# Kernel optimization log

Measured on AMD Instinct MI355X. Metric: run time of the kernel, lower is better.

The kernel has to match this reference:

```python
import jax, jax.numpy as jnp
import numpy as np

N, E, D = 50000, 800000, 256   # nodes, edges, hidden_dim
H, B, A = 8, 4, 3              # num_heads, num_bases, num_aggregators (symnorm,sum,max)
F = D // H                      # per-head width = bases feature width
G = 64                          # number of graphs in the batch
EPS = 1e-5                      # GraphNorm eps


def setup_inputs() -> dict:
    key = jax.random.key(0)
    ks = jax.random.split(key, 8)
    glorot = lambda k, shape: jax.random.normal(k, shape, jnp.float32) * np.sqrt(2.0 / (shape[0] + shape[1])).astype(np.float32)
    return {
        "node": jax.random.normal(ks[0], (N, D), jnp.float32),
        "edge_attr": jax.random.normal(ks[1], (E, 1), jnp.float32),  # unused by layer, kept for signature fidelity
        "W_bases": glorot(ks[2], (D, B * F)),                 # EGConv bases linear (no bias)
        "W_comb": glorot(ks[3], (D, H * B * A)),              # EGConv combination-weight linear
        "b_comb": jnp.zeros((H * B * A,), jnp.float32),
        "conv_bias": jnp.zeros((D,), jnp.float32),
        "gn_weight": jnp.ones((D,), jnp.float32),             # GraphNorm gamma
        "gn_bias": jnp.zeros((D,), jnp.float32),              # GraphNorm beta
        "gn_mean_scale": jnp.ones((D,), jnp.float32),         # GraphNorm alpha
        "edge_index": jax.random.randint(ks[4], (2, E), 0, N, dtype=jnp.int32),
        "batch": jnp.sort(jax.random.randint(ks[5], (N,), 0, G, dtype=jnp.int32)),
    }


def _forward(node, W_bases, W_comb, b_comb, conv_bias, gn_weight, gn_bias, gn_mean_scale, edge_index, batch):
    n = node.shape[0]
    loops = jnp.arange(n, dtype=edge_index.dtype)
    src = jnp.concatenate([edge_index[0], loops])  # add self-loops (EGConv add_self_loops=True / gcn_norm)
    dst = jnp.concatenate([edge_index[1], loops])

    # gcn_norm symmetric weights deg^-1/2[src] * deg^-1/2[dst]
    deg = jax.ops.segment_sum(jnp.ones_like(src, dtype=node.dtype), dst, num_segments=n)
    dinv = jnp.where(deg > 0, jax.lax.rsqrt(deg), 0.0)
    sym_w = dinv[src] * dinv[dst]

    bases = node @ W_bases            # [N, B*F]
    comb = node @ W_comb + b_comb     # [N, H*B*A]

    msg = bases[src]                  # [E+N, B*F] edge gather (dominant traffic)
    agg_sym = jax.ops.segment_sum(msg * sym_w[:, None], dst, num_segments=n)
    agg_sum = jax.ops.segment_sum(msg, dst, num_segments=n)
    agg_max = jax.ops.segment_max(msg, dst, num_segments=n)  # self-loops guarantee non-empty segments

    aggregated = jnp.stack([agg_sym, agg_sum, agg_max], axis=1)       # [N, A, B*F]
    aggregated = aggregated.reshape(n, A * B, F)                      # (a,b) fused index, as in PyG view
    weightings = comb.reshape(n, H, B * A)
    h = jnp.einsum('nhk,nkf->nhf', weightings, aggregated).reshape(n, D) + conv_bias

    # GraphNorm: per-graph mean/var with learnable mean scale alpha
    counts = jnp.maximum(jax.ops.segment_sum(jnp.ones((n,), node.dtype), batch, num_segments=G), 1.0)
    mean = jax.ops.segment_sum(h, batch, num_segments=G) / counts[:, None]
    hc = h - gn_mean_scale * mean[batch]
    var = jax.ops.segment_sum(hc * hc, batch, num_segments=G) / counts[:, None]
    out = gn_weight * hc * jax.lax.rsqrt(var[batch] + EPS) + gn_bias
    return jax.nn.relu(out)


def reference(node, edge_attr, W_bases, W_comb, b_comb, conv_bias, gn_weight, gn_bias, gn_mean_scale, edge_index, batch):
    del edge_attr  # unused by EGConv_layer, present in the torch forward signature
    return _forward(node, W_bases, W_comb, b_comb, conv_bias, gn_weight, gn_bias, gn_mean_scale, edge_index, batch)
```

## Files before the change

### kernel.cpp

```cpp
#include <hip/hip_runtime.h>
#include <hip/hip_bf16.h>

#define NN 50000
#define EE 800000
#define DD 256
#define BF 128
#define HC 96
#define GG 64
#define NT 14
#define KCN 8
#define RC 98
#define RSH 9
#define RSZ 512
#define CC 256
#define CS 3125
#define CAP 10240
#define SL 8
#define STG 10752

typedef short s16x8 __attribute__((ext_vector_type(8)));
typedef float f32x4 __attribute__((ext_vector_type(4)));

static __device__ __forceinline__ float b2f(unsigned u) {
    unsigned x = u << 16;
    float f;
    __builtin_memcpy(&f, &x, 4);
    return f;
}
static __device__ __forceinline__ unsigned short f2b(float f) {
    unsigned x;
    __builtin_memcpy(&x, &f, 4);
    unsigned lsb = (x >> 16) & 1u;
    x += 0x7fffu + lsb;
    return (unsigned short)(x >> 16);
}
static __device__ __forceinline__ unsigned pack_trunc(float lo, float hi) {
    unsigned ulo, uhi;
    __builtin_memcpy(&ulo, &lo, 4);
    __builtin_memcpy(&uhi, &hi, 4);
    return (ulo >> 16) | (uhi & 0xffff0000u);
}

__global__ void k_setup(const unsigned short* node_u16, int* flag,
                        const void* bcomb, const void* cbias, const void* gw,
                        const void* gb, const void* gms,
                        float* bcombF, float* cbiasF, float* gwF, float* gbF, float* gmsF,
                        const int* batch, int* goff) {
    if (blockIdx.x == 0) {
        __shared__ int cnt;
        if (threadIdx.x == 0) cnt = 0;
        __syncthreads();
        int local = 0;
        #pragma unroll
        for (int j = 0; j < 4; j++) {
            int idx = 2 * (threadIdx.x * 4 + j);
            unsigned short u = node_u16[idx];
            int e = (u >> 7) & 0xFF;
            if (e < 100 || e > 140) local++;
        }
        atomicAdd(&cnt, local);
        __syncthreads();
        int isf = (cnt > 256) ? 1 : 0;
        if (threadIdx.x == 0) flag[0] = isf;
        int d = threadIdx.x;
        auto rd = [&](const void* p, int i) -> float {
            return isf ? ((const float*)p)[i] : b2f(((const unsigned short*)p)[i]);
        };
        if (d < HC) bcombF[d] = rd(bcomb, d);
        cbiasF[d] = rd(cbias, d);
        gwF[d] = rd(gw, d);
        gbF[d] = rd(gb, d);
        gmsF[d] = rd(gms, d);
    } else {
        int g = threadIdx.x;
        if (g > GG) return;
        int lo = 0, hi = NN;
        while (lo < hi) { int mid = (lo + hi) >> 1; if (batch[mid] < g) lo = mid + 1; else hi = mid; }
        goff[g] = lo;
    }
}

__global__ __launch_bounds__(256) void k_cnt(const int* ei, int* cntg) {
    __shared__ int cnt[RC];
    int c = blockIdx.x, t = threadIdx.x;
    if (t < RC) cnt[t] = 0;
    __syncthreads();
    const int* dstp = ei + EE + (size_t)c * CS;
    for (int i = t; i < CS; i += 256) atomicAdd(&cnt[dstp[i] >> RSH], 1);
    __syncthreads();
    if (t < RC) cntg[c * RC + t] = cnt[t];
}

__global__ __launch_bounds__(256) void k_cscan(const int* cntg, int* baseg, int* cntr) {
    __shared__ int lds[256];
    int r = blockIdx.x, t = threadIdx.x;
    int v = cntg[t * RC + r];
    lds[t] = v;
    __syncthreads();
    for (int ofs = 1; ofs < 256; ofs <<= 1) {
        int add = (t >= ofs) ? lds[t - ofs] : 0;
        __syncthreads();
        lds[t] += add;
        __syncthreads();
    }
    baseg[t * RC + r] = r * CAP + lds[t] - v;
    if (t == 255) cntr[r] = lds[255];
}

__global__ void k_rscan(const int* cntr, int* rbase, int* row_off) {
    __shared__ int lds[128];
    int t = threadIdx.x;
    int nr = (t < RC) ? ((t == RC - 1) ? (NN - (RC - 1) * RSZ) : RSZ) : 0;
    int v = (t < RC) ? cntr[t] + nr : 0;
    lds[t] = v;
    __syncthreads();
    for (int ofs = 1; ofs < 128; ofs <<= 1) {
        int add = (t >= ofs) ? lds[t - ofs] : 0;
        __syncthreads();
        lds[t] += add;
        __syncthreads();
    }
    if (t < RC) rbase[t] = lds[t] - v;
    if (t == RC - 1) row_off[NN] = lds[t];
}

__global__ __launch_bounds__(256) void k_bucket(const int* ei, const int* baseg, unsigned* bucket) {
    __shared__ int cur[RC];
    int c = blockIdx.x, t = threadIdx.x;
    if (t < RC) cur[t] = baseg[c * RC + t];
    __syncthreads();
    const int* srcp = ei + (size_t)c * CS;
    const int* dstp = ei + EE + (size_t)c * CS;
    for (int i = t; i < CS; i += 256) {
        int d = dstp[i], s = srcp[i];
        int r = d >> RSH;
        int pos = atomicAdd(&cur[r], 1);
        bucket[pos] = ((unsigned)s << RSH) | (unsigned)(d & (RSZ - 1));
    }
}

__global__ __launch_bounds__(256) void k_build(const unsigned* bucket, const int* cntr,
                                               const int* rbase, int* row_off, float* dinv,
                                               int* csr) {
    __shared__ int hist[RSZ];
    __shared__ int stage[STG];
    __shared__ int scanbuf[256];
    int r = blockIdx.x, t = threadIdx.x;
    int n0 = r * RSZ;
    int nr = NN - n0; if (nr > RSZ) nr = RSZ;
    int cr = cntr[r];
    int rb = rbase[r];
    const unsigned* bk = bucket + (size_t)r * CAP;
    #pragma unroll
    for (int j = 0; j < 2; j++) hist[t + j * 256] = 0;
    __syncthreads();
    for (int i = t; i < cr; i += 256) atomicAdd(&hist[bk[i] & (RSZ - 1)], 1);
    __syncthreads();
    int a0 = (2 * t     < nr) ? hist[2 * t] + 1     : 0;
    int a1 = (2 * t + 1 < nr) ? hist[2 * t + 1] + 1 : 0;
    int s = a0 + a1;
    scanbuf[t] = s;
    __syncthreads();
    for (int ofs = 1; ofs < 256; ofs <<= 1) {
        int add = (t >= ofs) ? scanbuf[t - ofs] : 0;
        __syncthreads();
        scanbuf[t] += add;
        __syncthreads();
    }
    int excl = scanbuf[t] - s;
    int total = scanbuf[255];
    __syncthreads();
    if (2 * t < nr) {
        int n = 2 * t;
        row_off[n0 + n] = rb + excl;
        dinv[n0 + n] = rsqrtf((float)a0);
        stage[excl] = n0 + n;
        hist[n] = excl + 1;
    }
    if (2 * t + 1 < nr) {
        int n = 2 * t + 1;
        int e1 = excl + a0;
        row_off[n0 + n] = rb + e1;
        dinv[n0 + n] = rsqrtf((float)a1);
        stage[e1] = n0 + n;
        hist[n] = e1 + 1;
    }
    __syncthreads();
    for (int i = t; i < cr; i += 256) {
        unsigned p = bk[i];
        int slot = atomicAdd(&hist[p & (RSZ - 1)], 1);
        stage[slot] = (int)(p >> RSH);
    }
    __syncthreads();
    for (int i = t; i < total; i += 256) csr[rb + i] = stage[i];
}

__global__ void k_pack(const int* flag, const void* Wb, const void* Wc, unsigned short* wpack) {
    int t = blockIdx.x, kc = blockIdx.y, lane = threadIdx.x;
    int isf = flag[0];
    int n = t * 16 + (lane & 15);
    int kb = kc * 32 + (lane >> 4) * 8;
    unsigned short* o = wpack + (size_t)(((t * KCN) + kc) * 64 + lane) * 8;
    #pragma unroll
    for (int j = 0; j < 8; j++) {
        int k = kb + j;
        int src = (n < BF) ? (k * BF + n) : (k * HC + (n - BF));
        const void* W = (n < BF) ? Wb : Wc;
        o[j] = isf ? f2b(((const float*)W)[src]) : ((const unsigned short*)W)[src];
    }
}

__global__ __launch_bounds__(256) void k_gemm(const int* flag, const void* node,
                                              const unsigned short* wpack, const float* bcombF,
                                              unsigned short* bases, float* comb) {
    int wv = threadIdx.x >> 6, lane = threadIdx.x & 63;
    int row0 = blockIdx.x * 64 + wv * 16;
    int m = row0 + (lane & 15);
    int mc = m < NN ? m : NN - 1;
    int kg = lane >> 4;
    int isf = flag[0];
    const s16x8* bp = reinterpret_cast<const s16x8*>(wpack);
    f32x4 acc[NT];
    #pragma unroll
    for (int t = 0; t < NT; t++) acc[t] = (f32x4){0.f, 0.f, 0.f, 0.f};
    if (isf) {
        const float* nf = (const float*)node + (size_t)mc * DD;
        for (int kc = 0; kc < KCN; kc++) {
            const f32x4* src = reinterpret_cast<const f32x4*>(nf + kc * 32 + kg * 8);
            f32x4 x0 = src[0], x1 = src[1];
            union { s16x8 v; unsigned u[4]; } a;
            a.u[0] = pack_trunc(x0[0], x0[1]);
            a.u[1] = pack_trunc(x0[2], x0[3]);
            a.u[2] = pack_trunc(x1[0], x1[1]);
            a.u[3] = pack_trunc(x1[2], x1[3]);
            #pragma unroll
            for (int t = 0; t < NT; t++) {
                s16x8 b = bp[(size_t)(t * KCN + kc) * 64 + lane];
                acc[t] = __builtin_amdgcn_mfma_f32_16x16x32_bf16(a.v, b, acc[t], 0, 0, 0);
            }
        }
    } else {
        const s16x8* ap = reinterpret_cast<const s16x8*>(node);
        for (int kc = 0; kc < KCN; kc++) {
            s16x8 a = ap[(size_t)mc * 32 + kc * 4 + kg];
            #pragma unroll
            for (int t = 0; t < NT; t++) {
                s16x8 b = bp[(size_t)(t * KCN + kc) * 64 + lane];
                acc[t] = __builtin_amdgcn_mfma_f32_16x16x32_bf16(a, b, acc[t], 0, 0, 0);
            }
        }
    }
    int colb = lane & 15;
    #pragma unroll
    for (int t = 0; t < NT; t++) {
        int nc = t * 16 + colb;
        #pragma unroll
        for (int i = 0; i < 4; i++) {
            int r = row0 + kg * 4 + i;
            if (r < NN) {
                float v = acc[t][i];
                if (nc < BF) bases[(size_t)r * BF + nc] = f2b(v);
                else comb[(size_t)r * HC + (nc - BF)] = v + bcombF[nc - BF];
            }
        }
    }
}

__global__ __launch_bounds__(256) void k_agg(const unsigned short* bases,
                                             const float* comb, const float* dinv,
                                             const int* row_off, const int* csr,
                                             const float* cbiasF, unsigned short* h) {
    __shared__ float2 lds[4][3][64];
    int wv = threadIdx.x >> 6, lane = threadIdx.x & 63;
    int v = blockIdx.x * 4 + wv;
    int r0 = row_off[v], r1 = row_off[v + 1];
    float dv = dinv[v];
    const unsigned* bp = reinterpret_cast<const unsigned*>(bases);
    float sy0 = 0.f, sy1 = 0.f, su0 = 0.f, su1 = 0.f;
    float mx0 = -3.4e38f, mx1 = -3.4e38f;
    for (int base = r0; base < r1; base += 64) {
        int nload = r1 - base; if (nload > 64) nload = 64;
        int sidx = 0; float wgt = 0.f;
        if (lane < nload) { sidx = csr[base + lane]; wgt = dinv[sidx] * dv; }
        int j = 0;
        for (; j + 4 <= nload; j += 4) {
            int s0 = __shfl(sidx, j),     s1 = __shfl(sidx, j + 1);
            int s2 = __shfl(sidx, j + 2), s3 = __shfl(sidx, j + 3);
            float w0 = __shfl(wgt, j),     w1 = __shfl(wgt, j + 1);
            float w2 = __shfl(wgt, j + 2), w3 = __shfl(wgt, j + 3);
            unsigned g0 = bp[(size_t)s0 * 64 + lane];
            unsigned g1 = bp[(size_t)s1 * 64 + lane];
            unsigned g2 = bp[(size_t)s2 * 64 + lane];
            unsigned g3 = bp[(size_t)s3 * 64 + lane];
            float a, b;
            a = b2f(g0 & 0xffffu); b = b2f(g0 >> 16);
            sy0 += w0 * a; sy1 += w0 * b; su0 += a; su1 += b; mx0 = fmaxf(mx0, a); mx1 = fmaxf(mx1, b);
            a = b2f(g1 & 0xffffu); b = b2f(g1 >> 16);
            sy0 += w1 * a; sy1 += w1 * b; su0 += a; su1 += b; mx0 = fmaxf(mx0, a); mx1 = fmaxf(mx1, b);
            a = b2f(g2 & 0xffffu); b = b2f(g2 >> 16);
            sy0 += w2 * a; sy1 += w2 * b; su0 += a; su1 += b; mx0 = fmaxf(mx0, a); mx1 = fmaxf(mx1, b);
            a = b2f(g3 & 0xffffu); b = b2f(g3 >> 16);
            sy0 += w3 * a; sy1 += w3 * b; su0 += a; su1 += b; mx0 = fmaxf(mx0, a); mx1 = fmaxf(mx1, b);
        }
        for (; j < nload; j++) {
            int s0 = __shfl(sidx, j); float w0 = __shfl(wgt, j);
            unsigned g0 = bp[(size_t)s0 * 64 + lane];
            float a = b2f(g0 & 0xffffu), b = b2f(g0 >> 16);
            sy0 += w0 * a; sy1 += w0 * b; su0 += a; su1 += b; mx0 = fmaxf(mx0, a); mx1 = fmaxf(mx1, b);
        }
    }
    lds[wv][0][lane] = (float2){sy0, sy1};
    lds[wv][1][lane] = (float2){su0, su1};
    lds[wv][2][lane] = (float2){mx0, mx1};
    __syncthreads();
    const float* P0 = (const float*)&lds[wv][0][0];
    const float* P1 = (const float*)&lds[wv][1][0];
    const float* P2 = (const float*)&lds[wv][2][0];
    int d0 = lane * 4;
    int hh = d0 >> 5;
    float cb[12];
    #pragma unroll
    for (int k = 0; k < 12; k++) cb[k] = comb[(size_t)v * HC + hh * 12 + k];
    union { unsigned short e[4]; uint2 u; } o;
    #pragma unroll
    for (int i = 0; i < 4; i++) {
        int d = d0 + i, f = d & 31;
        float acc = cbiasF[d];
        #pragma unroll
        for (int k = 0; k < 12; k++) {
            int a = k >> 2, b = k & 3;
            const float* P = (a == 0) ? P0 : ((a == 1) ? P1 : P2);
            acc += cb[k] * P[b * 32 + f];
        }
        o.e[i] = f2b(acc);
    }
    reinterpret_cast<uint2*>(h)[(size_t)v * 64 + lane] = o.u;
}

__global__ void k_stats1(const unsigned short* h, const int* goff, float* sstat) {
    int g = blockIdx.x, s = blockIdx.y, t = threadIdx.x;
    int v0 = goff[g], v1 = goff[g + 1];
    float sum = 0.f, sq = 0.f;
    for (int v = v0 + s; v < v1; v += SL) {
        float x = b2f(h[(size_t)v * DD + t]);
        sum += x; sq += x * x;
    }
    size_t o = ((size_t)(g * SL + s)) * (2 * DD);
    sstat[o + t] = sum;
    sstat[o + DD + t] = sq;
}

__global__ void k_stats2(const float* sstat, const int* goff,
                         const float* gwF, const float* gbF, const float* gmsF,
                         float* sA, float* sB) {
    int g = blockIdx.x, d = threadIdx.x;
    float sum = 0.f, sq = 0.f;
    #pragma unroll
    for (int s = 0; s < SL; s++) {
        size_t o = ((size_t)(g * SL + s)) * (2 * DD);
        sum += sstat[o + d];
        sq  += sstat[o + DD + d];
    }
    int c = goff[g + 1] - goff[g];
    float cnt = (float)(c > 1 ? c : 1);
    float mu = sum / cnt;
    float m2 = sq / cnt;
    float al = gmsF[d];
    float var = m2 - mu * mu * (2.f * al - al * al);
    float rstd = rsqrtf(var + 1e-5f);
    float sa = gwF[d] * rstd;
    sA[g * DD + d] = sa;
    sB[g * DD + d] = gbF[d] - sa * al * mu;
}

__global__ void k_out(const int* flag, const unsigned short* h, const int* batch,
                      const float* sA, const float* sB, void* out) {
    int tid = blockIdx.x * 256 + threadIdx.x;
    int v = tid >> 6, q = tid & 63;
    if (v >= NN) return;
    int g = batch[v];
    uint2 xr = reinterpret_cast<const uint2*>(h)[(size_t)v * 64 + q];
    f32x4 a = reinterpret_cast<const f32x4*>(sA)[g * 64 + q];
    f32x4 b = reinterpret_cast<const f32x4*>(sB)[g * 64 + q];
    float x0 = b2f(xr.x & 0xffffu), x1 = b2f(xr.x >> 16);
    float x2 = b2f(xr.y & 0xffffu), x3 = b2f(xr.y >> 16);
    float y0 = fmaxf(x0 * a[0] + b[0], 0.f);
    float y1 = fmaxf(x1 * a[1] + b[1], 0.f);
    float y2 = fmaxf(x2 * a[2] + b[2], 0.f);
    float y3 = fmaxf(x3 * a[3] + b[3], 0.f);
    if (flag[0]) {
        f32x4 y = {y0, y1, y2, y3};
        reinterpret_cast<f32x4*>(out)[(size_t)v * 64 + q] = y;
    } else {
        union { unsigned short e[4]; uint2 u; } o;
        o.e[0] = f2b(y0); o.e[1] = f2b(y1); o.e[2] = f2b(y2); o.e[3] = f2b(y3);
        reinterpret_cast<uint2*>(out)[(size_t)v * 64 + q] = o.u;
    }
}

extern "C" void kernel_launch(void* const* d_in, const int* in_sizes, int n_in,
                              void* d_out, int out_size, void* d_ws, size_t ws_size,
                              hipStream_t stream) {
    const void* node  = d_in[0];
    const void* Wb    = d_in[2];
    const void* Wc    = d_in[3];
    const void* bcomb = d_in[4];
    const void* cbias = d_in[5];
    const void* gw    = d_in[6];
    const void* gb    = d_in[7];
    const void* gms   = d_in[8];
    const int* ei     = (const int*)d_in[9];
    const int* batch  = (const int*)d_in[10];

    char* w = (char*)d_ws;
    size_t off = 0;
    auto alloc = [&](size_t bytes) -> void* {
        off = (off + 255) & ~(size_t)255;
        void* p = w + off;
        off += bytes;
        return p;
    };
    unsigned short* bases = (unsigned short*)alloc((size_t)NN * BF * 2);
    float* comb    = (float*)alloc((size_t)NN * HC * 4);
    unsigned short* h = (unsigned short*)alloc((size_t)NN * DD * 2);
    int*   csr     = (int*)alloc((size_t)(EE + NN) * 4);
    unsigned* bucket = (unsigned*)alloc((size_t)RC * CAP * 4);
    int*   cntg    = (int*)alloc((size_t)CC * RC * 4);
    int*   baseg   = (int*)alloc((size_t)CC * RC * 4);
    int*   cntrr   = (int*)alloc((size_t)RC * 4);
    int*   rbase   = (int*)alloc((size_t)RC * 4);
    float* dinv    = (float*)alloc((size_t)NN * 4);
    int*   row_off = (int*)alloc((size_t)(NN + 1) * 4);
    int*   goff    = (int*)alloc((size_t)(GG + 1) * 4);
    float* sstat   = (float*)alloc((size_t)GG * SL * 2 * DD * 4);
    float* sA      = (float*)alloc((size_t)GG * DD * 4);
    float* sB      = (float*)alloc((size_t)GG * DD * 4);
    unsigned short* wpack = (unsigned short*)alloc((size_t)NT * KCN * 64 * 8 * 2);
    int*   flag    = (int*)alloc(256);
    float* bcombF  = (float*)alloc(HC * 4);
    float* cbiasF  = (float*)alloc(DD * 4);
    float* gwF     = (float*)alloc(DD * 4);
    float* gbF     = (float*)alloc(DD * 4);
    float* gmsF    = (float*)alloc(DD * 4);

    k_setup<<<2, 256, 0, stream>>>((const unsigned short*)node, flag, bcomb, cbias, gw, gb, gms,
                                   bcombF, cbiasF, gwF, gbF, gmsF, batch, goff);
    k_cnt<<<CC, 256, 0, stream>>>(ei, cntg);
    k_cscan<<<RC, 256, 0, stream>>>(cntg, baseg, cntrr);
    k_rscan<<<1, 128, 0, stream>>>(cntrr, rbase, row_off);
    k_bucket<<<CC, 256, 0, stream>>>(ei, baseg, bucket);
    k_build<<<RC, 256, 0, stream>>>(bucket, cntrr, rbase, row_off, dinv, csr);
    k_pack<<<dim3(NT, KCN), 64, 0, stream>>>(flag, Wb, Wc, wpack);
    k_gemm<<<(NN + 63) / 64, 256, 0, stream>>>(flag, node, wpack, bcombF, bases, comb);
    k_agg<<<NN / 4, 256, 0, stream>>>(bases, comb, dinv, row_off, csr, cbiasF, h);
    k_stats1<<<dim3(GG, SL), 256, 0, stream>>>(h, goff, sstat);
    k_stats2<<<GG, 256, 0, stream>>>(sstat, goff, gwF, gbF, gmsF, sA, sB);
    k_out<<<(NN * 64 + 255) / 256, 256, 0, stream>>>(flag, h, batch, sA, sB, d_out);
}
```

Measured before the change: 271.2 us.

## Retile GEMM across waves, widen gather unroll, vectorize GraphNorm stats

The GEMM kernel now gives each block 16 rows, with two waves each computing 7 of the 14 output column tiles. This cuts accumulator registers and raises the block count. The aggregation loop is unrolled to issue 8 independent row gathers before accumulating, which puts more memory loads in flight. The stats pass reads two bf16 values per thread with half as many threads, and the graph split factor is doubled to 16 for more parallelism. The row bounds checks are dropped because N divides evenly by 16. The node A-tile is now loaded twice per block, once per wave.

New measurement: 267.9 us. No clear change (-1.2%).

```diff
diff --git a/kernel.cpp b/kernel.cpp
--- a/kernel.cpp
+++ b/kernel.cpp
@@ -15,7 +15,7 @@
 #define CC 256
 #define CS 3125
 #define CAP 10240
-#define SL 8
+#define SL 16
 #define STG 10752
 
 typedef short s16x8 __attribute__((ext_vector_type(8)));
@@ -210,21 +210,19 @@
     }
 }
 
-__global__ __launch_bounds__(256) void k_gemm(const int* flag, const void* node,
+__global__ __launch_bounds__(128) void k_gemm(const int* flag, const void* node,
                                               const unsigned short* wpack, const float* bcombF,
                                               unsigned short* bases, float* comb) {
     int wv = threadIdx.x >> 6, lane = threadIdx.x & 63;
-    int row0 = blockIdx.x * 64 + wv * 16;
-    int m = row0 + (lane & 15);
-    int mc = m < NN ? m : NN - 1;
+    int m = blockIdx.x * 16 + (lane & 15);
     int kg = lane >> 4;
     int isf = flag[0];
     const s16x8* bp = reinterpret_cast<const s16x8*>(wpack);
-    f32x4 acc[NT];
-    #pragma unroll
-    for (int t = 0; t < NT; t++) acc[t] = (f32x4){0.f, 0.f, 0.f, 0.f};
+    f32x4 acc[7];
+    #pragma unroll
+    for (int t = 0; t < 7; t++) acc[t] = (f32x4){0.f, 0.f, 0.f, 0.f};
     if (isf) {
-        const float* nf = (const float*)node + (size_t)mc * DD;
+        const float* nf = (const float*)node + (size_t)m * DD;
         for (int kc = 0; kc < KCN; kc++) {
             const f32x4* src = reinterpret_cast<const f32x4*>(nf + kc * 32 + kg * 8);
             f32x4 x0 = src[0], x1 = src[1];
@@ -234,34 +232,35 @@
             a.u[2] = pack_trunc(x1[0], x1[1]);
             a.u[3] = pack_trunc(x1[2], x1[3]);
             #pragma unroll
-            for (int t = 0; t < NT; t++) {
+            for (int t2 = 0; t2 < 7; t2++) {
+                int t = wv * 7 + t2;
                 s16x8 b = bp[(size_t)(t * KCN + kc) * 64 + lane];
-                acc[t] = __builtin_amdgcn_mfma_f32_16x16x32_bf16(a.v, b, acc[t], 0, 0, 0);
+                acc[t2] = __builtin_amdgcn_mfma_f32_16x16x32_bf16(a.v, b, acc[t2], 0, 0, 0);
             }
         }
     } else {
         const s16x8* ap = reinterpret_cast<const s16x8*>(node);
         for (int kc = 0; kc < KCN; kc++) {
-            s16x8 a = ap[(size_t)mc * 32 + kc * 4 + kg];
+            s16x8 a = ap[(size_t)m * 32 + kc * 4 + kg];
             #pragma unroll
-            for (int t = 0; t < NT; t++) {
+            for (int t2 = 0; t2 < 7; t2++) {
+                int t = wv * 7 + t2;
                 s16x8 b = bp[(size_t)(t * KCN + kc) * 64 + lane];
-                acc[t] = __builtin_amdgcn_mfma_f32_16x16x32_bf16(a, b, acc[t], 0, 0, 0);
+                acc[t2] = __builtin_amdgcn_mfma_f32_16x16x32_bf16(a, b, acc[t2], 0, 0, 0);
             }
         }
     }
     int colb = lane & 15;
-    #pragma unroll
-    for (int t = 0; t < NT; t++) {
-        int nc = t * 16 + colb;
+    int row0 = blockIdx.x * 16;
+    #pragma unroll
+    for (int t2 = 0; t2 < 7; t2++) {
+        int nc = (wv * 7 + t2) * 16 + colb;
         #pragma unroll
         for (int i = 0; i < 4; i++) {
             int r = row0 + kg * 4 + i;
-            if (r < NN) {
-                float v = acc[t][i];
-                if (nc < BF) bases[(size_t)r * BF + nc] = f2b(v);
-                else comb[(size_t)r * HC + (nc - BF)] = v + bcombF[nc - BF];
-            }
+            float v = acc[t2][i];
+            if (nc < BF) bases[(size_t)r * BF + nc] = f2b(v);
+            else comb[(size_t)r * HC + (nc - BF)] = v + bcombF[nc - BF];
         }
     }
 }
@@ -283,24 +282,19 @@
         int sidx = 0; float wgt = 0.f;
         if (lane < nload) { sidx = csr[base + lane]; wgt = dinv[sidx] * dv; }
         int j = 0;
-        for (; j + 4 <= nload; j += 4) {
-            int s0 = __shfl(sidx, j),     s1 = __shfl(sidx, j + 1);
-            int s2 = __shfl(sidx, j + 2), s3 = __shfl(sidx, j + 3);
-            float w0 = __shfl(wgt, j),     w1 = __shfl(wgt, j + 1);
-            float w2 = __shfl(wgt, j + 2), w3 = __shfl(wgt, j + 3);
-            unsigned g0 = bp[(size_t)s0 * 64 + lane];
-            unsigned g1 = bp[(size_t)s1 * 64 + lane];
-            unsigned g2 = bp[(size_t)s2 * 64 + lane];
-            unsigned g3 = bp[(size_t)s3 * 64 + lane];
-            float a, b;
-            a = b2f(g0 & 0xffffu); b = b2f(g0 >> 16);
-            sy0 += w0 * a; sy1 += w0 * b; su0 += a; su1 += b; mx0 = fmaxf(mx0, a); mx1 = fmaxf(mx1, b);
-            a = b2f(g1 & 0xffffu); b = b2f(g1 >> 16);
-            sy0 += w1 * a; sy1 += w1 * b; su0 += a; su1 += b; mx0 = fmaxf(mx0, a); mx1 = fmaxf(mx1, b);
-            a = b2f(g2 & 0xffffu); b = b2f(g2 >> 16);
-            sy0 += w2 * a; sy1 += w2 * b; su0 += a; su1 += b; mx0 = fmaxf(mx0, a); mx1 = fmaxf(mx1, b);
-            a = b2f(g3 & 0xffffu); b = b2f(g3 >> 16);
-            sy0 += w3 * a; sy1 += w3 * b; su0 += a; su1 += b; mx0 = fmaxf(mx0, a); mx1 = fmaxf(mx1, b);
+        for (; j + 8 <= nload; j += 8) {
+            int ss[8]; float ww[8]; unsigned gg[8];
+            #pragma unroll
+            for (int k = 0; k < 8; k++) { ss[k] = __shfl(sidx, j + k); ww[k] = __shfl(wgt, j + k); }
+            #pragma unroll
+            for (int k = 0; k < 8; k++) gg[k] = bp[(size_t)ss[k] * 64 + lane];
+            #pragma unroll
+            for (int k = 0; k < 8; k++) {
+                float a = b2f(gg[k] & 0xffffu), b = b2f(gg[k] >> 16);
+                sy0 += ww[k] * a; sy1 += ww[k] * b;
+                su0 += a; su1 += b;
+                mx0 = fmaxf(mx0, a); mx1 = fmaxf(mx1, b);
+            }
         }
         for (; j < nload; j++) {
             int s0 = __shfl(sidx, j); float w0 = __shfl(wgt, j);
@@ -337,17 +331,21 @@
     reinterpret_cast<uint2*>(h)[(size_t)v * 64 + lane] = o.u;
 }
 
-__global__ void k_stats1(const unsigned short* h, const int* goff, float* sstat) {
+__global__ __launch_bounds__(128) void k_stats1(const unsigned short* h, const int* goff, float* sstat) {
     int g = blockIdx.x, s = blockIdx.y, t = threadIdx.x;
     int v0 = goff[g], v1 = goff[g + 1];
-    float sum = 0.f, sq = 0.f;
+    const unsigned* hu = reinterpret_cast<const unsigned*>(h);
+    float s0 = 0.f, s1 = 0.f, q0 = 0.f, q1 = 0.f;
     for (int v = v0 + s; v < v1; v += SL) {
-        float x = b2f(h[(size_t)v * DD + t]);
-        sum += x; sq += x * x;
+        unsigned x = hu[(size_t)v * 128 + t];
+        float a = b2f(x & 0xffffu), b = b2f(x >> 16);
+        s0 += a; s1 += b; q0 += a * a; q1 += b * b;
     }
     size_t o = ((size_t)(g * SL + s)) * (2 * DD);
-    sstat[o + t] = sum;
-    sstat[o + DD + t] = sq;
+    sstat[o + 2 * t] = s0;
+    sstat[o + 2 * t + 1] = s1;
+    sstat[o + DD + 2 * t] = q0;
+    sstat[o + DD + 2 * t + 1] = q1;
 }
 
 __global__ void k_stats2(const float* sstat, const int* goff,
@@ -355,7 +353,6 @@
                          float* sA, float* sB) {
     int g = blockIdx.x, d = threadIdx.x;
     float sum = 0.f, sq = 0.f;
-    #pragma unroll
     for (int s = 0; s < SL; s++) {
         size_t o = ((size_t)(g * SL + s)) * (2 * DD);
         sum += sstat[o + d];
@@ -451,9 +448,9 @@
     k_bucket<<<CC, 256, 0, stream>>>(ei, baseg, bucket);
     k_build<<<RC, 256, 0, stream>>>(bucket, cntrr, rbase, row_off, dinv, csr);
     k_pack<<<dim3(NT, KCN), 64, 0, stream>>>(flag, Wb, Wc, wpack);
-    k_gemm<<<(NN + 63) / 64, 256, 0, stream>>>(flag, node, wpack, bcombF, bases, comb);
+    k_gemm<<<NN / 16, 128, 0, stream>>>(flag, node, wpack, bcombF, bases, comb);
     k_agg<<<NN / 4, 256, 0, stream>>>(bases, comb, dinv, row_off, csr, cbiasF, h);
-    k_stats1<<<dim3(GG, SL), 256, 0, stream>>>(h, goff, sstat);
+    k_stats1<<<dim3(GG, SL), 128, 0, stream>>>(h, goff, sstat);
     k_stats2<<<GG, 256, 0, stream>>>(sstat, goff, gwF, gbF, gmsF, sA, sB);
     k_out<<<(NN * 64 + 255) / 256, 256, 0, stream>>>(flag, h, batch, sA, sB, d_out);
 }
```
